# Kernel tuning notes

Hardware: AMD Instinct MI355X
Metric: run time of the kernel (lower is better)

Reference implementation:

```python
import jax, jax.numpy as jnp
import numpy as np

_WINDOW = 2  # len_sort_window in the torch module


def _butterfly_indices(L, D):
    """Replicates get_butterfly_matrix's index columns.

    Column 0 is arange(L). Each subsequent column d (1-indexed) is arange(L)
    rolled right by shift_offset, where shift_offset starts at 0 and increases
    by 2 per column (mod L). The butterfly_factor_to_matrix result is computed
    but never used in the original code, so it is omitted here.
    Result[i, d] = (i - shift_d) mod L.
    """
    shifts = np.concatenate([[0], (_WINDOW * np.arange(D - 1)) % L])  # [D]
    idx = (np.arange(L)[:, None] - shifts[None, :]) % L  # [L, D]
    return jnp.asarray(idx, dtype=jnp.int32)


def setup_inputs() -> dict:
    key = jax.random.key(0)
    v = jax.random.normal(key, (16, 16384, 128), dtype=jnp.float32)
    return {"v": v}


def reference(v):
    B, L, D = v.shape  # static under jit
    idx = _butterfly_indices(L, D)  # [L, D]
    # v_shifted[b, i, d] = v[b, idx[i, d], d]  (torch.gather along dim 1)
    v_shifted = jnp.take_along_axis(v, jnp.broadcast_to(idx[None], (B, L, D)), axis=1)
    # window-2 ascending sort == compare-exchange (min, max)
    vw = v_shifted.reshape(B, L // _WINDOW, _WINDOW, D)
    lo = jnp.minimum(vw[:, :, 0], vw[:, :, 1])
    hi = jnp.maximum(vw[:, :, 0], vw[:, :, 1])
    out = jnp.stack([lo, hi], axis=2).reshape(B, L, D)
    return out
```

## Files before the change

### kernel.cpp

```cpp
#include <hip/hip_runtime.h>
#include <cstdint>
#include <cstddef>

#define L_DIM 16384
#define D_DIM 128
#define B_DIM 16

#define TR 512
#define DG 32
#define HALO 64
#define ROWS (TR + HALO)
#define NSWEEP (ROWS / 64)

__global__ __launch_bounds__(512, 2) void butterfly_reg_kernel(
    const float* __restrict__ v, float* __restrict__ out) {
  __shared__ float lds[ROWS * DG];

  const int rtile = blockIdx.x;
  const int g     = blockIdx.y;
  const int b     = blockIdx.z;
  const int r0    = rtile * TR;
  const int d0    = g * DG;
  const int smax  = 64 * g + 60;
  const int rin0  = r0 - smax;

  const int t = threadIdx.x;

  const float* vb = v   + (size_t)b * (L_DIM * D_DIM);
  float*       ob = out + (size_t)b * (L_DIM * D_DIM);

  const int srow  = t >> 3;
  const int scol4 = t & 7;
  float4 stg[NSWEEP];
#pragma unroll
  for (int s = 0; s < NSWEEP; ++s) {
    const int rt   = s * 64 + srow;
    const int grow = (rin0 + rt) & (L_DIM - 1);
    stg[s] = *reinterpret_cast<const float4*>(
        vb + (size_t)grow * D_DIM + d0 + scol4 * 4);
  }
#pragma unroll
  for (int s = 0; s < NSWEEP; ++s) {
    const int rt = s * 64 + srow;
    *reinterpret_cast<float4*>(&lds[rt * DG + scol4 * 4]) = stg[s];
  }
  __syncthreads();

  const int c  = t & 31;
  const int sg = t >> 5;
  const int d  = d0 + c;
  const int s_d  = (d == 0) ? 0 : (2 * d - 2);
  const int boff = smax - s_d;

#pragma unroll
  for (int kk = 0; kk < TR / 32; ++kk) {
    const int pr = kk * 16 + sg;
    const int lr = 2 * pr + boff;
    const float a0 = lds[lr * DG + c];
    const float a1 = lds[(lr + 1) * DG + c];
    const float lo = fminf(a0, a1);
    const float hi = fmaxf(a0, a1);
    float* op = ob + (size_t)(r0 + 2 * pr) * D_DIM + d;
    op[0]     = lo;
    op[D_DIM] = hi;
  }
}

extern "C" void kernel_launch(void* const* d_in, const int* in_sizes, int n_in,
                              void* d_out, int out_size, void* d_ws, size_t ws_size,
                              hipStream_t stream) {
  const float* v = (const float*)d_in[0];
  float* out = (float*)d_out;
  dim3 grid(L_DIM / TR, D_DIM / DG, B_DIM);
  dim3 block(512);
  butterfly_reg_kernel<<<grid, block, 0, stream>>>(v, out);
}
```

Baseline: 229.4 us.

## Stream full-width row chunks through an LDS ring buffer with register prefetch

Replaces the per-tile kernel, which staged a 512-row by 32-column tile plus a halo, with 256 persistent-style blocks. Each block covers a 1024-row chunk at all 128 columns and streams 64-row batches through a 320-row circular LDS buffer, prefetching the next batch into registers while the current one is computed. This removes the redundant halo reads (each column group previously reloaded up to 64 extra rows per tile) and overlaps global loads with compute. The costs are lower parallelism (256 blocks of one wave-group each), a barrier per batch, and a mapped block order meant to spread chunks across XCDs.

```diff
diff --git a/kernel.cpp b/kernel.cpp
--- a/kernel.cpp
+++ b/kernel.cpp
@@ -6,63 +6,98 @@
 #define D_DIM 128
 #define B_DIM 16
 
-#define TR 512
-#define DG 32
-#define HALO 64
-#define ROWS (TR + HALO)
-#define NSWEEP (ROWS / 64)
+#define TPB 512
+#define CHUNK 1024
+#define BATCH 64
+#define RING 320
+#define NB_OUT (CHUNK / BATCH)
 
-__global__ __launch_bounds__(512, 2) void butterfly_reg_kernel(
+__global__ __launch_bounds__(TPB) void butterfly_dense_kernel(
     const float* __restrict__ v, float* __restrict__ out) {
-  __shared__ float lds[ROWS * DG];
+  __shared__ float lds[RING * D_DIM];
 
-  const int rtile = blockIdx.x;
-  const int g     = blockIdx.y;
-  const int b     = blockIdx.z;
-  const int r0    = rtile * TR;
-  const int d0    = g * DG;
-  const int smax  = 64 * g + 60;
-  const int rin0  = r0 - smax;
+  const int blk = blockIdx.x;
+  const int x = blk & 7, y = blk >> 3;
+  const int b  = y >> 1;
+  const int ch = 2 * x + (y & 1);
+  const int R0  = ch * CHUNK;
+  const int IN0 = R0 - 256 + L_DIM;
 
   const int t = threadIdx.x;
 
   const float* vb = v   + (size_t)b * (L_DIM * D_DIM);
   float*       ob = out + (size_t)b * (L_DIM * D_DIM);
 
-  const int srow  = t >> 3;
-  const int scol4 = t & 7;
-  float4 stg[NSWEEP];
+  const int srow = t >> 5;
+  const int sc4  = (t & 31) * 4;
+
+  float4 pre[16];
 #pragma unroll
-  for (int s = 0; s < NSWEEP; ++s) {
-    const int rt   = s * 64 + srow;
-    const int grow = (rin0 + rt) & (L_DIM - 1);
-    stg[s] = *reinterpret_cast<const float4*>(
-        vb + (size_t)grow * D_DIM + d0 + scol4 * 4);
+  for (int i = 0; i < 16; ++i) {
+    const int bt = i >> 2, u = i & 3;
+    const int row  = bt * BATCH + u * 16 + srow;
+    const int grow = (IN0 + row) & (L_DIM - 1);
+    pre[i] = *reinterpret_cast<const float4*>(vb + (size_t)grow * D_DIM + sc4);
   }
 #pragma unroll
-  for (int s = 0; s < NSWEEP; ++s) {
-    const int rt = s * 64 + srow;
-    *reinterpret_cast<float4*>(&lds[rt * DG + scol4 * 4]) = stg[s];
+  for (int i = 0; i < 16; ++i) {
+    const int bt = i >> 2, u = i & 3;
+    const int row = bt * BATCH + u * 16 + srow;
+    *reinterpret_cast<float4*>(&lds[row * D_DIM + sc4]) = pre[i];
   }
-  __syncthreads();
+  float4 rg[2][4];
+#pragma unroll
+  for (int u = 0; u < 4; ++u) {
+    const int row  = 4 * BATCH + u * 16 + srow;
+    const int grow = (IN0 + row) & (L_DIM - 1);
+    rg[0][u] = *reinterpret_cast<const float4*>(vb + (size_t)grow * D_DIM + sc4);
+  }
+  asm volatile("s_waitcnt lgkmcnt(0)" ::: "memory");
+  __builtin_amdgcn_s_barrier();
 
-  const int c  = t & 31;
-  const int sg = t >> 5;
-  const int d  = d0 + c;
-  const int s_d  = (d == 0) ? 0 : (2 * d - 2);
-  const int boff = smax - s_d;
+  const int d   = t & 127;
+  const int pj  = t >> 7;
+  const int s_d = (d == 0) ? 0 : (2 * d - 2);
+  const int offb = 256 - s_d + 2 * pj;
 
 #pragma unroll
-  for (int kk = 0; kk < TR / 32; ++kk) {
-    const int pr = kk * 16 + sg;
-    const int lr = 2 * pr + boff;
-    const float a0 = lds[lr * DG + c];
-    const float a1 = lds[(lr + 1) * DG + c];
-    const float lo = fminf(a0, a1);
-    const float hi = fmaxf(a0, a1);
-    float* op = ob + (size_t)(r0 + 2 * pr) * D_DIM + d;
-    op[0]     = lo;
-    op[D_DIM] = hi;
+  for (int w = 0; w < NB_OUT; ++w) {
+    if (w < NB_OUT - 1) {
+#pragma unroll
+      for (int u = 0; u < 4; ++u) {
+        const int row  = (w + 5) * BATCH + u * 16 + srow;
+        const int grow = (IN0 + row) & (L_DIM - 1);
+        rg[(w + 1) & 1][u] =
+            *reinterpret_cast<const float4*>(vb + (size_t)grow * D_DIM + sc4);
+      }
+    }
+    {
+      const int slotbase = ((w + 4) % 5) * BATCH;
+#pragma unroll
+      for (int u = 0; u < 4; ++u) {
+        const int row = slotbase + u * 16 + srow;
+        *reinterpret_cast<float4*>(&lds[row * D_DIM + sc4]) = rg[w & 1][u];
+      }
+    }
+    asm volatile("s_waitcnt lgkmcnt(0)" ::: "memory");
+    __builtin_amdgcn_s_barrier();
+
+    const int base = (BATCH * w) % RING;
+    float* obw = ob + (size_t)(R0 + BATCH * w) * D_DIM + d;
+#pragma unroll
+    for (int s = 0; s < 8; ++s) {
+      int q0 = base + offb + 8 * s;
+      q0 = (q0 >= RING) ? q0 - RING : q0;
+      int q1 = q0 + 1;
+      q1 = (q1 >= RING) ? q1 - RING : q1;
+      const float a0 = lds[q0 * D_DIM + d];
+      const float a1 = lds[q1 * D_DIM + d];
+      const int orow = 8 * s + 2 * pj;
+      obw[(size_t)orow * D_DIM]       = fminf(a0, a1);
+      obw[(size_t)(orow + 1) * D_DIM] = fmaxf(a0, a1);
+    }
+    asm volatile("s_waitcnt lgkmcnt(0)" ::: "memory");
+    __builtin_amdgcn_s_barrier();
   }
 }
 
@@ -71,7 +106,7 @@
                               hipStream_t stream) {
   const float* v = (const float*)d_in[0];
   float* out = (float*)d_out;
-  dim3 grid(L_DIM / TR, D_DIM / DG, B_DIM);
-  dim3 block(512);
-  butterfly_reg_kernel<<<grid, block, 0, stream>>>(v, out);
+  dim3 grid(256);
+  dim3 block(TPB);
+  butterfly_dense_kernel<<<grid, block, 0, stream>>>(v, out);
 }
```

Result: slower. 256.2 us (+11.7%).
